# Optimization experiments

Measured on AMD Instinct MI355X. Metric: run time of the kernel, lower is better.

The kernel has to match this reference:

```python
import jax, jax.numpy as jnp
import numpy as np

CHARB_EPS = 1e-3
CHARB_ALPHA = 0.45
EDGE_ALPHA = 10.0
BOUNDARY_SUPPRESS = 0.1
W_SMOOTH = 0.15
W_SEGCONS = 0.1
SEG_EPS = 1e-6


def charbonnier(x):
    return jnp.power(x * x + CHARB_EPS * CHARB_EPS, CHARB_ALPHA)


def depthwise_sobel(img, kern):
    # img: (B,C,H,W); kern: (3,3) -> depthwise conv, padding=1
    C = img.shape[1]
    k = jnp.broadcast_to(kern[None, None], (C, 1, 3, 3)).astype(img.dtype)
    return jax.lax.conv_general_dilated(
        img, k, window_strides=(1, 1), padding=[(1, 1), (1, 1)],
        dimension_numbers=('NCHW', 'OIHW', 'NCHW'), feature_group_count=C)


def maxpool3(x):
    # 3x3 max pool, stride 1, pad 1 over last two dims (any rank)
    nd = x.ndim
    return jax.lax.reduce_window(
        x, -jnp.inf, jax.lax.max,
        (1,) * (nd - 2) + (3, 3), (1,) * nd,
        [(0, 0)] * (nd - 2) + [(1, 1), (1, 1)])


def compute_segment_boundary(masks):
    # masks: (B,S,H,W) -> boundary (B,1,H,W)
    occ = masks.sum(axis=1, keepdims=True)             # (B,1,H,W)
    b = jnp.clip(maxpool3(occ) - (-maxpool3(-occ)), 0.0, 1.0)
    per = jnp.clip(maxpool3(masks) - (-maxpool3(-masks)), 0.0, 1.0)  # (B,S,H,W)
    b = b + per.sum(axis=1, keepdims=True)
    return jnp.clip(b, 0.0, 1.0)


def boundary_smooth_loss(flow, image, segment_masks):
    sobel_x = jnp.array([[1., 0., -1.], [2., 0., -2.], [1., 0., -1.]], dtype=flow.dtype)
    gx = depthwise_sobel(image, sobel_x)
    gy = depthwise_sobel(image, sobel_x.T)
    img_grad_mag = (jnp.abs(gx) + jnp.abs(gy)).mean(axis=1, keepdims=True)  # (B,1,H,W)
    edge_w = jnp.exp(-EDGE_ALPHA * img_grad_mag)
    boundary = compute_segment_boundary(segment_masks)
    boundary_w = 1.0 - boundary * (1.0 - BOUNDARY_SUPPRESS)
    weights = edge_w * boundary_w                       # (B,1,H,W)

    fx = flow[:, :, :, 1:] - flow[:, :, :, :-1]
    fy = flow[:, :, 1:, :] - flow[:, :, :-1, :]
    wx = weights[:, :, :, 1:]
    wy = weights[:, :, 1:, :]
    loss1 = (charbonnier(fx).mean(axis=1, keepdims=True) * wx).mean()
    loss1 = loss1 + (charbonnier(fy).mean(axis=1, keepdims=True) * wy).mean()
    # second order
    fxx = fx[:, :, :, 1:] - fx[:, :, :, :-1]
    fyy = fy[:, :, 1:, :] - fy[:, :, :-1, :]
    loss2 = charbonnier(fxx).mean() + charbonnier(fyy).mean()
    return W_SMOOTH * (loss1 + 0.5 * loss2)


def segment_consistency_loss(flow, segment_masks):
    # flow: (B,2,H,W); masks: (B,S,H,W)
    mask_sum = jnp.maximum(segment_masks.sum(axis=(-2, -1)), SEG_EPS)  # (B,S)
    mean_flow = jnp.einsum('bchw,bshw->bsc', flow, segment_masks) / mask_sum[..., None]
    diff = flow[:, None] - mean_flow[:, :, :, None, None]              # (B,S,2,H,W)
    diff_sq = (diff * diff).sum(axis=2)                                # (B,S,H,W)
    # charbonnier(sqrt(d)) == (d + eps^2)^alpha (grad-safe at 0)
    var_map = jnp.power(diff_sq + CHARB_EPS * CHARB_EPS, CHARB_ALPHA)
    num_s = jnp.einsum('bshw,bshw->s', var_map, segment_masks)         # (S,)
    w_s = mask_sum.sum(axis=0)                                         # (S,)
    loss_s = num_s / jnp.maximum(w_s, SEG_EPS)
    total = (loss_s * w_s).sum()
    tw = w_s.sum()
    loss = jnp.where(tw > SEG_EPS, total / tw, 0.0)
    return W_SEGCONS * loss


def setup_inputs() -> dict:
    key = jax.random.key(0)
    k1, k2, k3 = jax.random.split(key, 3)
    B, S, H, W = 8, 16, 512, 512
    flow = jax.random.normal(k1, (B, 2, H, W), dtype=jnp.float32)
    image = jax.random.uniform(k2, (B, 3, H, W), dtype=jnp.float32)
    segment_masks = jax.random.uniform(k3, (B, S, H, W), dtype=jnp.float32)
    return {'flow': flow, 'image': image, 'segment_masks': segment_masks}


def reference(flow, image, segment_masks):
    return segment_consistency_loss(flow, segment_masks) + boundary_smooth_loss(flow, image, segment_masks)
```

## Files before the change

kernel.cpp:

```cpp
#include <hip/hip_runtime.h>

#define BB 8
#define SS 16
#define HH 512
#define WW 512
#define HWP (HH*WW)

#define TH 16
#define TW 32
#define HR 18
#define HC 34
#define NH (HR*HC)
#define LW 35

#define WS_MSUM 0
#define WS_FSUM 128
#define WS_MEAN 384
#define WS_ACC  640
#define WS_TOTAL 660

__device__ __forceinline__ float clip01(float x){ return fminf(fmaxf(x, 0.0f), 1.0f); }
__device__ __forceinline__ float pow045(float v){ return exp2f(0.45f * log2f(v)); }
__device__ __forceinline__ float cbn(float x){ return pow045(x*x + 1e-6f); }

__global__ __launch_bounds__(256, 2)
void kA(const float* __restrict__ flow, const float* __restrict__ masks,
        float* __restrict__ ws)
{
    const int b = blockIdx.y;
    const int base = blockIdx.x * 2048;
    const float* fU = flow + (size_t)b * 2 * HWP;
    const float* fV = fU + HWP;
    const float* mb = masks + (size_t)b * SS * HWP;

    float am[SS], au[SS], av[SS];
#pragma unroll
    for (int s = 0; s < SS; ++s){ am[s]=0.f; au[s]=0.f; av[s]=0.f; }

    for (int it = 0; it < 2; ++it){
        const int p = base + it*1024 + threadIdx.x*4;
        const float4 u = *reinterpret_cast<const float4*>(fU + p);
        const float4 v = *reinterpret_cast<const float4*>(fV + p);
#pragma unroll
        for (int s = 0; s < SS; ++s){
            const float4 m = *reinterpret_cast<const float4*>(mb + s*HWP + p);
            am[s] += (m.x + m.y) + (m.z + m.w);
            au[s] += m.x*u.x + m.y*u.y + m.z*u.z + m.w*u.w;
            av[s] += m.x*v.x + m.y*v.y + m.z*v.z + m.w*v.w;
        }
    }

#pragma unroll
    for (int s = 0; s < SS; ++s){
#pragma unroll
        for (int o = 32; o > 0; o >>= 1){
            am[s] += __shfl_down(am[s], o, 64);
            au[s] += __shfl_down(au[s], o, 64);
            av[s] += __shfl_down(av[s], o, 64);
        }
    }
    __shared__ float red[4][3*SS];
    const int lane = threadIdx.x & 63, wv = threadIdx.x >> 6;
    if (lane == 0){
#pragma unroll
        for (int s = 0; s < SS; ++s){
            red[wv][s] = am[s]; red[wv][SS+s] = au[s]; red[wv][2*SS+s] = av[s];
        }
    }
    __syncthreads();
    if (threadIdx.x < 3*SS){
        const int i = threadIdx.x;
        float t = red[0][i] + red[1][i] + red[2][i] + red[3][i];
        const int s = i % SS, kind = i / SS;
        if (kind == 0) atomicAdd(ws + WS_MSUM + b*SS + s, t);
        else           atomicAdd(ws + WS_FSUM + (b*SS + s)*2 + (kind-1), t);
    }
}

__global__ void kB(float* __restrict__ ws)
{
    const int i = threadIdx.x;
    const int bs = i >> 1;
    const float ms = fmaxf(ws[WS_MSUM + bs], 1e-6f);
    ws[WS_MEAN + i] = ws[WS_FSUM + i] / ms;
}

__global__ __launch_bounds__(256, 2)
void kC(const float* __restrict__ flow, const float* __restrict__ image,
        const float* __restrict__ masks, float* __restrict__ ws)
{
    const int b  = blockIdx.z;
    const int h0 = blockIdx.y * TH;
    const int w0 = blockIdx.x * TW;
    const int tid = threadIdx.x;

    __shared__ float sImg[3][HR*LW];
    __shared__ float sFlo[2][HR*LW];
    __shared__ float sOcc[HR*LW];
    __shared__ float sMsk[2][HR*LW];
    __shared__ float sMean[2*SS];
    __shared__ float sRed[4][20];

    if (tid < 2*SS) sMean[tid] = ws[WS_MEAN + b*2*SS + tid];

    int hli[3], cgi[3]; bool hval[3]; bool hin[3]; int hgi[3];
#pragma unroll
    for (int k = 0; k < 3; ++k){
        const int idx = tid + k*256;
        hval[k] = (k < 2) || (tid < NH - 512);
        const int r = idx / HC, c = idx % HC;
        const int gh = h0 - 1 + r, gw = w0 - 1 + c;
        hli[k] = r*LW + c;
        hin[k] = ((unsigned)gh < (unsigned)HH) && ((unsigned)gw < (unsigned)WW);
        hgi[k] = gh*WW + gw;
        const int ch_ = min(max(gh, 0), HH-1);
        const int cw_ = min(max(gw, 0), WW-1);
        cgi[k] = ch_*WW + cw_;
    }

    const float* img = image + (size_t)b * 3 * HWP;
    const float* flo = flow  + (size_t)b * 2 * HWP;
    const float* mb  = masks + (size_t)b * SS * HWP;

#pragma unroll
    for (int k = 0; k < 3; ++k){
        if (hval[k]){
            const bool in = hin[k]; const int gi = hgi[k]; const int li = hli[k];
            sImg[0][li] = in ? img[0*HWP + gi] : 0.f;
            sImg[1][li] = in ? img[1*HWP + gi] : 0.f;
            sImg[2][li] = in ? img[2*HWP + gi] : 0.f;
            sFlo[0][li] = in ? flo[0*HWP + gi] : 0.f;
            sFlo[1][li] = in ? flo[1*HWP + gi] : 0.f;
        }
    }

    float occA[3] = {0.f, 0.f, 0.f};
    float pf[3];

#pragma unroll
    for (int k = 0; k < 3; ++k) if (hval[k]) pf[k] = mb[cgi[k]];
#pragma unroll
    for (int k = 0; k < 3; ++k) if (hval[k]){ sMsk[0][hli[k]] = pf[k]; occA[k] += pf[k]; }
#pragma unroll
    for (int k = 0; k < 3; ++k) if (hval[k]) pf[k] = mb[1*HWP + cgi[k]];
    __syncthreads();

    const int pr  = tid >> 4;
    const int pc2 = (tid & 15) << 1;
    const int R = pr + 1;
    const float fu0 = sFlo[0][R*LW + pc2+1], fu1 = sFlo[0][R*LW + pc2+2];
    const float fv0 = sFlo[1][R*LW + pc2+1], fv1 = sFlo[1][R*LW + pc2+2];

    float numv[SS];
    float perS0 = 0.f, perS1 = 0.f;

#pragma unroll
    for (int s = 0; s < SS; ++s){
        const float* bufc = sMsk[s & 1];
        float cmx[4], cmn[4], mC0 = 0.f, mC1 = 0.f;
#pragma unroll
        for (int j = 0; j < 4; ++j){
            const float a = bufc[(pr  )*LW + pc2 + j];
            const float m = bufc[(pr+1)*LW + pc2 + j];
            const float d = bufc[(pr+2)*LW + pc2 + j];
            cmx[j] = fmaxf(fmaxf(a, m), d);
            cmn[j] = fminf(fminf(a, m), d);
            if (j == 1) mC0 = m;
            if (j == 2) mC1 = m;
        }
        const float rng0 = fmaxf(fmaxf(cmx[0],cmx[1]),cmx[2]) - fminf(fminf(cmn[0],cmn[1]),cmn[2]);
        const float rng1 = fmaxf(fmaxf(cmx[1],cmx[2]),cmx[3]) - fminf(fminf(cmn[1],cmn[2]),cmn[3]);
        perS0 += clip01(rng0);
        perS1 += clip01(rng1);

        const float mu = sMean[2*s], mv = sMean[2*s+1];
        const float d0u = fu0-mu, d0v = fv0-mv, d1u = fu1-mu, d1v = fv1-mv;
        const float vm0 = pow045(d0u*d0u + d0v*d0v + 1e-6f);
        const float vm1 = pow045(d1u*d1u + d1v*d1v + 1e-6f);
        numv[s] = vm0*mC0 + vm1*mC1;

        if (s < SS-1){
#pragma unroll
            for (int k = 0; k < 3; ++k) if (hval[k]){ sMsk[(s+1)&1][hli[k]] = pf[k]; occA[k] += pf[k]; }
            if (s < SS-2){
#pragma unroll
                for (int k = 0; k < 3; ++k) if (hval[k]) pf[k] = mb[(s+2)*HWP + cgi[k]];
            }
            __syncthreads();
        }
    }

#pragma unroll
    for (int k = 0; k < 3; ++k) if (hval[k]) sOcc[hli[k]] = occA[k];
    __syncthreads();

    float ox[4], on[4];
#pragma unroll
    for (int j = 0; j < 4; ++j){
        const float a = sOcc[(pr  )*LW + pc2 + j];
        const float m = sOcc[(pr+1)*LW + pc2 + j];
        const float d = sOcc[(pr+2)*LW + pc2 + j];
        ox[j] = fmaxf(fmaxf(a, m), d);
        on[j] = fminf(fminf(a, m), d);
    }
    const float org0 = fmaxf(fmaxf(ox[0],ox[1]),ox[2]) - fminf(fminf(on[0],on[1]),on[2]);
    const float org1 = fmaxf(fmaxf(ox[1],ox[2]),ox[3]) - fminf(fminf(on[1],on[2]),on[3]);
    const float bnd0 = clip01(clip01(org0) + perS0);
    const float bnd1 = clip01(clip01(org1) + perS1);

    float mag0 = 0.f, mag1 = 0.f;
#pragma unroll
    for (int ch = 0; ch < 3; ++ch){
        float top[4], mid[4], bot[4];
#pragma unroll
        for (int j = 0; j < 4; ++j){
            top[j] = sImg[ch][(pr  )*LW + pc2 + j];
            mid[j] = sImg[ch][(pr+1)*LW + pc2 + j];
            bot[j] = sImg[ch][(pr+2)*LW + pc2 + j];
        }
        float colV0 = top[0] + 2.f*mid[0] + bot[0];
        float colV1 = top[1] + 2.f*mid[1] + bot[1];
        float colV2 = top[2] + 2.f*mid[2] + bot[2];
        float colV3 = top[3] + 2.f*mid[3] + bot[3];
        const float gx0 = colV0 - colV2;
        const float gx1 = colV1 - colV3;
        const float gy0 = (top[0] + 2.f*top[1] + top[2]) - (bot[0] + 2.f*bot[1] + bot[2]);
        const float gy1 = (top[1] + 2.f*top[2] + top[3]) - (bot[1] + 2.f*bot[2] + bot[3]);
        mag0 += fabsf(gx0) + fabsf(gy0);
        mag1 += fabsf(gx1) + fabsf(gy1);
    }
    mag0 *= (1.f/3.f); mag1 *= (1.f/3.f);
    const float wgt0 = expf(-10.f * mag0) * (1.f - 0.9f*bnd0);
    const float wgt1 = expf(-10.f * mag1) * (1.f - 0.9f*bnd1);

    const int gh  = h0 + pr;
    const int gw0 = w0 + pc2;
    const int gw1 = gw0 + 1;

    const float lu = sFlo[0][R*LW + pc2],     lv = sFlo[1][R*LW + pc2];
    const float ru = sFlo[0][R*LW + pc2 + 3], rv = sFlo[1][R*LW + pc2 + 3];
    const float uu0 = sFlo[0][(R-1)*LW + pc2+1], uv0 = sFlo[1][(R-1)*LW + pc2+1];
    const float uu1 = sFlo[0][(R-1)*LW + pc2+2], uv1 = sFlo[1][(R-1)*LW + pc2+2];
    const float du0 = sFlo[0][(R+1)*LW + pc2+1], dv0 = sFlo[1][(R+1)*LW + pc2+1];
    const float du1 = sFlo[0][(R+1)*LW + pc2+2], dv1 = sFlo[1][(R+1)*LW + pc2+2];

    float l1x = 0.f, l1y = 0.f, l2x = 0.f, l2y = 0.f;

    if (gw0 >= 1) l1x += 0.5f * (cbn(fu0 - lu) + cbn(fv0 - lv)) * wgt0;
    l1x += 0.5f * (cbn(fu1 - fu0) + cbn(fv1 - fv0)) * wgt1;
    if (gh >= 1){
        l1y += 0.5f * (cbn(fu0 - uu0) + cbn(fv0 - uv0)) * wgt0;
        l1y += 0.5f * (cbn(fu1 - uu1) + cbn(fv1 - uv1)) * wgt1;
    }
    if (gw0 >= 1) l2x += cbn(fu1 - 2.f*fu0 + lu) + cbn(fv1 - 2.f*fv0 + lv);
    if (gw1 <= WW-2) l2x += cbn(ru - 2.f*fu1 + fu0) + cbn(rv - 2.f*fv1 + fv0);
    if (gh >= 1 && gh <= HH-2){
        l2y += cbn(du0 - 2.f*fu0 + uu0) + cbn(dv0 - 2.f*fv0 + uv0);
        l2y += cbn(du1 - 2.f*fu1 + uu1) + cbn(dv1 - 2.f*fv1 + uv1);
    }

    float vals[20];
#pragma unroll
    for (int s = 0; s < SS; ++s) vals[s] = numv[s];
    vals[16] = l1x; vals[17] = l1y; vals[18] = l2x; vals[19] = l2y;

    const int lane = tid & 63, wv = tid >> 6;
#pragma unroll
    for (int i = 0; i < 20; ++i){
        float v = vals[i];
#pragma unroll
        for (int o = 32; o > 0; o >>= 1) v += __shfl_down(v, o, 64);
        if (lane == 0) sRed[wv][i] = v;
    }
    __syncthreads();
    if (tid < 20){
        const float t = sRed[0][tid] + sRed[1][tid] + sRed[2][tid] + sRed[3][tid];
        atomicAdd(ws + WS_ACC + tid, t);
    }
}

__global__ void kF(const float* __restrict__ ws, float* __restrict__ out)
{
    __shared__ float sw[SS];
    const int t = threadIdx.x;
    if (t < SS){
        float w = 0.f;
        for (int b = 0; b < BB; ++b) w += fmaxf(ws[WS_MSUM + b*SS + t], 1e-6f);
        sw[t] = w;
    }
    __syncthreads();
    if (t == 0){
        float total = 0.f, tw = 0.f;
        for (int s = 0; s < SS; ++s){
            const float w = sw[s];
            total += (ws[WS_ACC + s] / fmaxf(w, 1e-6f)) * w;
            tw += w;
        }
        const float seg = (tw > 1e-6f) ? (total / tw) : 0.f;
        const float l1 = ws[WS_ACC+16] / (8.f*512.f*511.f) + ws[WS_ACC+17] / (8.f*511.f*512.f);
        const float l2 = ws[WS_ACC+18] / (8.f*2.f*512.f*510.f) + ws[WS_ACC+19] / (8.f*2.f*510.f*512.f);
        out[0] = 0.1f*seg + 0.15f*(l1 + 0.5f*l2);
    }
}

extern "C" void kernel_launch(void* const* d_in, const int* in_sizes, int n_in,
                              void* d_out, int out_size, void* d_ws, size_t ws_size,
                              hipStream_t stream)
{
    (void)in_sizes; (void)n_in; (void)out_size; (void)ws_size;
    const float* flow  = (const float*)d_in[0];
    const float* image = (const float*)d_in[1];
    const float* masks = (const float*)d_in[2];
    float* ws  = (float*)d_ws;
    float* out = (float*)d_out;

    (void)hipMemsetAsync(d_ws, 0, WS_TOTAL * sizeof(float), stream);

    dim3 gA(128, BB);
    kA<<<gA, 256, 0, stream>>>(flow, masks, ws);
    kB<<<1, 256, 0, stream>>>(ws);
    dim3 gC(WW/TW, HH/TH, BB);
    kC<<<gC, 256, 0, stream>>>(flow, image, masks, ws);
    kF<<<1, 64, 0, stream>>>(ws, out);
}
```

Before: 376.8 us.

## Pipeline kA through LDS async loads, drop kB, and remove shared tiling in kC

kA now streams masks and flow into double-buffered LDS using global_load_lds async copies, with fewer, larger blocks. kB's mean computation is folded into kC's prologue, removing one launch. kC drops its shared-memory halo tiles and per-segment barriers. Each thread instead handles one column over two rows and reads its 3x4 neighbourhood straight from global memory, relying on caches for the halo reuse. This removes sync overhead and LDS traffic, at the cost of more redundant global and cache reads.

```diff
diff --git a/kernel.cpp b/kernel.cpp
--- a/kernel.cpp
+++ b/kernel.cpp
@@ -6,16 +6,8 @@
 #define WW 512
 #define HWP (HH*WW)
 
-#define TH 16
-#define TW 32
-#define HR 18
-#define HC 34
-#define NH (HR*HC)
-#define LW 35
-
 #define WS_MSUM 0
 #define WS_FSUM 128
-#define WS_MEAN 384
 #define WS_ACC  640
 #define WS_TOTAL 660
 
@@ -23,31 +15,65 @@
 __device__ __forceinline__ float pow045(float v){ return exp2f(0.45f * log2f(v)); }
 __device__ __forceinline__ float cbn(float x){ return pow045(x*x + 1e-6f); }
 
-__global__ __launch_bounds__(256, 2)
+typedef const __attribute__((address_space(1))) void* as1cv;
+typedef __attribute__((address_space(3))) void* as3v;
+__device__ __forceinline__ void gload16(const void* g, void* l){
+    __builtin_amdgcn_global_load_lds((as1cv)g, (as3v)l, 16, 0, 0);
+}
+
+__global__ __launch_bounds__(256)
 void kA(const float* __restrict__ flow, const float* __restrict__ masks,
         float* __restrict__ ws)
 {
-    const int b = blockIdx.y;
-    const int base = blockIdx.x * 2048;
+    const int b   = blockIdx.y;
+    const int tb0 = blockIdx.x * 4096;
     const float* fU = flow + (size_t)b * 2 * HWP;
     const float* fV = fU + HWP;
     const float* mb = masks + (size_t)b * SS * HWP;
 
+    __shared__ float buf[2][36*256];
+    __shared__ float red[4][3*SS];
+
+    const int wv = threadIdx.x >> 6, lane = threadIdx.x & 63;
+
     float am[SS], au[SS], av[SS];
 #pragma unroll
     for (int s = 0; s < SS; ++s){ am[s]=0.f; au[s]=0.f; av[s]=0.f; }
 
-    for (int it = 0; it < 2; ++it){
-        const int p = base + it*1024 + threadIdx.x*4;
-        const float4 u = *reinterpret_cast<const float4*>(fU + p);
-        const float4 v = *reinterpret_cast<const float4*>(fV + p);
+    auto stage = [&](int t, int pb){
+        const int tb = tb0 + t * 512;
+        float* base = &buf[pb][0];
+#pragma unroll
+        for (int k = 0; k < 9; ++k){
+            const int c = wv + 4*k;
+            const float* src;
+            if (c < 32)       src = mb + (size_t)(c>>1)*HWP + tb + (c&1)*256;
+            else if (c < 34)  src = fU + tb + (c&1)*256;
+            else              src = fV + tb + (c&1)*256;
+            gload16(src + lane*4, base + c*256);
+        }
+    };
+
+    auto compute = [&](int pb){
+        const float* B = &buf[pb][0];
+        const int t2 = threadIdx.x * 2;
+        const float2 uu = *reinterpret_cast<const float2*>(B + 16*512 + t2);
+        const float2 vv = *reinterpret_cast<const float2*>(B + 16*512 + 512 + t2);
 #pragma unroll
         for (int s = 0; s < SS; ++s){
-            const float4 m = *reinterpret_cast<const float4*>(mb + s*HWP + p);
-            am[s] += (m.x + m.y) + (m.z + m.w);
-            au[s] += m.x*u.x + m.y*u.y + m.z*u.z + m.w*u.w;
-            av[s] += m.x*v.x + m.y*v.y + m.z*v.z + m.w*v.w;
-        }
+            const float2 m = *reinterpret_cast<const float2*>(B + s*512 + t2);
+            am[s] += m.x + m.y;
+            au[s] += m.x*uu.x + m.y*uu.y;
+            av[s] += m.x*vv.x + m.y*vv.y;
+        }
+    };
+
+    stage(0, 0);
+    __syncthreads();
+    for (int t = 0; t < 8; ++t){
+        if (t < 7) stage(t+1, (t+1)&1);
+        compute(t & 1);
+        __syncthreads();
     }
 
 #pragma unroll
@@ -59,8 +85,6 @@
             av[s] += __shfl_down(av[s], o, 64);
         }
     }
-    __shared__ float red[4][3*SS];
-    const int lane = threadIdx.x & 63, wv = threadIdx.x >> 6;
     if (lane == 0){
 #pragma unroll
         for (int s = 0; s < SS; ++s){
@@ -70,207 +94,148 @@
     __syncthreads();
     if (threadIdx.x < 3*SS){
         const int i = threadIdx.x;
-        float t = red[0][i] + red[1][i] + red[2][i] + red[3][i];
+        const float t = red[0][i] + red[1][i] + red[2][i] + red[3][i];
         const int s = i % SS, kind = i / SS;
         if (kind == 0) atomicAdd(ws + WS_MSUM + b*SS + s, t);
         else           atomicAdd(ws + WS_FSUM + (b*SS + s)*2 + (kind-1), t);
     }
 }
 
-__global__ void kB(float* __restrict__ ws)
-{
-    const int i = threadIdx.x;
-    const int bs = i >> 1;
-    const float ms = fmaxf(ws[WS_MSUM + bs], 1e-6f);
-    ws[WS_MEAN + i] = ws[WS_FSUM + i] / ms;
-}
-
-__global__ __launch_bounds__(256, 2)
+__global__ __launch_bounds__(256)
 void kC(const float* __restrict__ flow, const float* __restrict__ image,
         const float* __restrict__ masks, float* __restrict__ ws)
 {
     const int b  = blockIdx.z;
-    const int h0 = blockIdx.y * TH;
-    const int w0 = blockIdx.x * TW;
     const int tid = threadIdx.x;
-
-    __shared__ float sImg[3][HR*LW];
-    __shared__ float sFlo[2][HR*LW];
-    __shared__ float sOcc[HR*LW];
-    __shared__ float sMsk[2][HR*LW];
+    const int h0 = blockIdx.y*16 + ((tid>>5)<<1);
+    const int w  = blockIdx.x*32 + (tid&31);
+
     __shared__ float sMean[2*SS];
     __shared__ float sRed[4][20];
-
-    if (tid < 2*SS) sMean[tid] = ws[WS_MEAN + b*2*SS + tid];
-
-    int hli[3], cgi[3]; bool hval[3]; bool hin[3]; int hgi[3];
-#pragma unroll
-    for (int k = 0; k < 3; ++k){
-        const int idx = tid + k*256;
-        hval[k] = (k < 2) || (tid < NH - 512);
-        const int r = idx / HC, c = idx % HC;
-        const int gh = h0 - 1 + r, gw = w0 - 1 + c;
-        hli[k] = r*LW + c;
-        hin[k] = ((unsigned)gh < (unsigned)HH) && ((unsigned)gw < (unsigned)WW);
-        hgi[k] = gh*WW + gw;
-        const int ch_ = min(max(gh, 0), HH-1);
-        const int cw_ = min(max(gw, 0), WW-1);
-        cgi[k] = ch_*WW + cw_;
-    }
-
+    if (tid < 2*SS){
+        const int s = tid >> 1;
+        const float ms = fmaxf(ws[WS_MSUM + b*SS + s], 1e-6f);
+        sMean[tid] = ws[WS_FSUM + (b*SS + s)*2 + (tid&1)] / ms;
+    }
+    __syncthreads();
+
+    const int rA = max(h0-1, 0), rC = h0+1, rD = min(h0+2, HH-1);
+    const int wm = max(w-1, 0),  wp = min(w+1, WW-1);
+    const int oA = rA*WW, oB = h0*WW, oC = rC*WW, oD = rD*WW;
+
+    const float* mb  = masks + (size_t)b * SS * HWP;
+    const float* flo = flow  + (size_t)b * 2 * HWP;
     const float* img = image + (size_t)b * 3 * HWP;
-    const float* flo = flow  + (size_t)b * 2 * HWP;
-    const float* mb  = masks + (size_t)b * SS * HWP;
-
-#pragma unroll
-    for (int k = 0; k < 3; ++k){
-        if (hval[k]){
-            const bool in = hin[k]; const int gi = hgi[k]; const int li = hli[k];
-            sImg[0][li] = in ? img[0*HWP + gi] : 0.f;
-            sImg[1][li] = in ? img[1*HWP + gi] : 0.f;
-            sImg[2][li] = in ? img[2*HWP + gi] : 0.f;
-            sFlo[0][li] = in ? flo[0*HWP + gi] : 0.f;
-            sFlo[1][li] = in ? flo[1*HWP + gi] : 0.f;
-        }
-    }
-
-    float occA[3] = {0.f, 0.f, 0.f};
-    float pf[3];
-
-#pragma unroll
-    for (int k = 0; k < 3; ++k) if (hval[k]) pf[k] = mb[cgi[k]];
-#pragma unroll
-    for (int k = 0; k < 3; ++k) if (hval[k]){ sMsk[0][hli[k]] = pf[k]; occA[k] += pf[k]; }
-#pragma unroll
-    for (int k = 0; k < 3; ++k) if (hval[k]) pf[k] = mb[1*HWP + cgi[k]];
-    __syncthreads();
-
-    const int pr  = tid >> 4;
-    const int pc2 = (tid & 15) << 1;
-    const int R = pr + 1;
-    const float fu0 = sFlo[0][R*LW + pc2+1], fu1 = sFlo[0][R*LW + pc2+2];
-    const float fv0 = sFlo[1][R*LW + pc2+1], fv1 = sFlo[1][R*LW + pc2+2];
-
+
+    const float fu0 = flo[oB + w],       fu1 = flo[oC + w];
+    const float fv0 = flo[HWP + oB + w], fv1 = flo[HWP + oC + w];
+
+    float occ[12];
+#pragma unroll
+    for (int j = 0; j < 12; ++j) occ[j] = 0.f;
     float numv[SS];
     float perS0 = 0.f, perS1 = 0.f;
 
 #pragma unroll
     for (int s = 0; s < SS; ++s){
-        const float* bufc = sMsk[s & 1];
-        float cmx[4], cmn[4], mC0 = 0.f, mC1 = 0.f;
-#pragma unroll
-        for (int j = 0; j < 4; ++j){
-            const float a = bufc[(pr  )*LW + pc2 + j];
-            const float m = bufc[(pr+1)*LW + pc2 + j];
-            const float d = bufc[(pr+2)*LW + pc2 + j];
-            cmx[j] = fmaxf(fmaxf(a, m), d);
-            cmn[j] = fminf(fminf(a, m), d);
-            if (j == 1) mC0 = m;
-            if (j == 2) mC1 = m;
-        }
-        const float rng0 = fmaxf(fmaxf(cmx[0],cmx[1]),cmx[2]) - fminf(fminf(cmn[0],cmn[1]),cmn[2]);
-        const float rng1 = fmaxf(fmaxf(cmx[1],cmx[2]),cmx[3]) - fminf(fminf(cmn[1],cmn[2]),cmn[3]);
+        const float* M = mb + (size_t)s * HWP;
+        const float mAm=M[oA+wm], mA0=M[oA+w], mAp=M[oA+wp];
+        const float mBm=M[oB+wm], mB0=M[oB+w], mBp=M[oB+wp];
+        const float mCm=M[oC+wm], mC0=M[oC+w], mCp=M[oC+wp];
+        const float mDm=M[oD+wm], mD0=M[oD+w], mDp=M[oD+wp];
+        occ[0]+=mAm; occ[1]+=mA0;  occ[2]+=mAp;
+        occ[3]+=mBm; occ[4]+=mB0;  occ[5]+=mBp;
+        occ[6]+=mCm; occ[7]+=mC0;  occ[8]+=mCp;
+        occ[9]+=mDm; occ[10]+=mD0; occ[11]+=mDp;
+
+        const float xm = fmaxf(mBm,mCm), x0 = fmaxf(mB0,mC0), xp = fmaxf(mBp,mCp);
+        const float nm = fminf(mBm,mCm), n0 = fminf(mB0,mC0), np = fminf(mBp,mCp);
+        const float rng0 = fmaxf(fmaxf(fmaxf(xm,mAm), fmaxf(x0,mA0)), fmaxf(xp,mAp))
+                         - fminf(fminf(fminf(nm,mAm), fminf(n0,mA0)), fminf(np,mAp));
+        const float rng1 = fmaxf(fmaxf(fmaxf(xm,mDm), fmaxf(x0,mD0)), fmaxf(xp,mDp))
+                         - fminf(fminf(fminf(nm,mDm), fminf(n0,mD0)), fminf(np,mDp));
         perS0 += clip01(rng0);
         perS1 += clip01(rng1);
 
         const float mu = sMean[2*s], mv = sMean[2*s+1];
         const float d0u = fu0-mu, d0v = fv0-mv, d1u = fu1-mu, d1v = fv1-mv;
-        const float vm0 = pow045(d0u*d0u + d0v*d0v + 1e-6f);
-        const float vm1 = pow045(d1u*d1u + d1v*d1v + 1e-6f);
-        numv[s] = vm0*mC0 + vm1*mC1;
-
-        if (s < SS-1){
-#pragma unroll
-            for (int k = 0; k < 3; ++k) if (hval[k]){ sMsk[(s+1)&1][hli[k]] = pf[k]; occA[k] += pf[k]; }
-            if (s < SS-2){
-#pragma unroll
-                for (int k = 0; k < 3; ++k) if (hval[k]) pf[k] = mb[(s+2)*HWP + cgi[k]];
-            }
-            __syncthreads();
-        }
-    }
-
-#pragma unroll
-    for (int k = 0; k < 3; ++k) if (hval[k]) sOcc[hli[k]] = occA[k];
-    __syncthreads();
-
-    float ox[4], on[4];
-#pragma unroll
-    for (int j = 0; j < 4; ++j){
-        const float a = sOcc[(pr  )*LW + pc2 + j];
-        const float m = sOcc[(pr+1)*LW + pc2 + j];
-        const float d = sOcc[(pr+2)*LW + pc2 + j];
-        ox[j] = fmaxf(fmaxf(a, m), d);
-        on[j] = fminf(fminf(a, m), d);
-    }
-    const float org0 = fmaxf(fmaxf(ox[0],ox[1]),ox[2]) - fminf(fminf(on[0],on[1]),on[2]);
-    const float org1 = fmaxf(fmaxf(ox[1],ox[2]),ox[3]) - fminf(fminf(on[1],on[2]),on[3]);
+        numv[s] = pow045(d0u*d0u + d0v*d0v + 1e-6f)*mB0
+                + pow045(d1u*d1u + d1v*d1v + 1e-6f)*mC0;
+    }
+
+    const float oxm = fmaxf(occ[3],occ[6]), ox0 = fmaxf(occ[4],occ[7]), oxp = fmaxf(occ[5],occ[8]);
+    const float onm = fminf(occ[3],occ[6]), on0 = fminf(occ[4],occ[7]), onp = fminf(occ[5],occ[8]);
+    const float org0 = fmaxf(fmaxf(fmaxf(oxm,occ[0]), fmaxf(ox0,occ[1])), fmaxf(oxp,occ[2]))
+                     - fminf(fminf(fminf(onm,occ[0]), fminf(on0,occ[1])), fminf(onp,occ[2]));
+    const float org1 = fmaxf(fmaxf(fmaxf(oxm,occ[9]), fmaxf(ox0,occ[10])), fmaxf(oxp,occ[11]))
+                     - fminf(fminf(fminf(onm,occ[9]), fminf(on0,occ[10])), fminf(onp,occ[11]));
     const float bnd0 = clip01(clip01(org0) + perS0);
     const float bnd1 = clip01(clip01(org1) + perS1);
 
+    const bool vA = (h0 >= 1), vD = (h0+2 <= HH-1);
+    const bool vm = (w  >= 1), vp = (w+1  <= WW-1);
     float mag0 = 0.f, mag1 = 0.f;
 #pragma unroll
     for (int ch = 0; ch < 3; ++ch){
-        float top[4], mid[4], bot[4];
-#pragma unroll
-        for (int j = 0; j < 4; ++j){
-            top[j] = sImg[ch][(pr  )*LW + pc2 + j];
-            mid[j] = sImg[ch][(pr+1)*LW + pc2 + j];
-            bot[j] = sImg[ch][(pr+2)*LW + pc2 + j];
-        }
-        float colV0 = top[0] + 2.f*mid[0] + bot[0];
-        float colV1 = top[1] + 2.f*mid[1] + bot[1];
-        float colV2 = top[2] + 2.f*mid[2] + bot[2];
-        float colV3 = top[3] + 2.f*mid[3] + bot[3];
-        const float gx0 = colV0 - colV2;
-        const float gx1 = colV1 - colV3;
-        const float gy0 = (top[0] + 2.f*top[1] + top[2]) - (bot[0] + 2.f*bot[1] + bot[2]);
-        const float gy1 = (top[1] + 2.f*top[2] + top[3]) - (bot[1] + 2.f*bot[2] + bot[3]);
+        const float* I = img + (size_t)ch * HWP;
+        const float iAm = (vA&&vm) ? I[oA+wm] : 0.f;
+        const float iA0 =  vA      ? I[oA+w ] : 0.f;
+        const float iAp = (vA&&vp) ? I[oA+wp] : 0.f;
+        const float iBm =  vm      ? I[oB+wm] : 0.f;
+        const float iB0 =             I[oB+w ];
+        const float iBp =  vp      ? I[oB+wp] : 0.f;
+        const float iCm =  vm      ? I[oC+wm] : 0.f;
+        const float iC0 =             I[oC+w ];
+        const float iCp =  vp      ? I[oC+wp] : 0.f;
+        const float iDm = (vD&&vm) ? I[oD+wm] : 0.f;
+        const float iD0 =  vD      ? I[oD+w ] : 0.f;
+        const float iDp = (vD&&vp) ? I[oD+wp] : 0.f;
+
+        const float gx0 = (iAm + 2.f*iBm + iCm) - (iAp + 2.f*iBp + iCp);
+        const float gy0 = (iAm + 2.f*iA0 + iAp) - (iCm + 2.f*iC0 + iCp);
         mag0 += fabsf(gx0) + fabsf(gy0);
+        const float gx1 = (iBm + 2.f*iCm + iDm) - (iBp + 2.f*iCp + iDp);
+        const float gy1 = (iBm + 2.f*iB0 + iBp) - (iDm + 2.f*iD0 + iDp);
         mag1 += fabsf(gx1) + fabsf(gy1);
     }
     mag0 *= (1.f/3.f); mag1 *= (1.f/3.f);
     const float wgt0 = expf(-10.f * mag0) * (1.f - 0.9f*bnd0);
     const float wgt1 = expf(-10.f * mag1) * (1.f - 0.9f*bnd1);
 
-    const int gh  = h0 + pr;
-    const int gw0 = w0 + pc2;
-    const int gw1 = gw0 + 1;
-
-    const float lu = sFlo[0][R*LW + pc2],     lv = sFlo[1][R*LW + pc2];
-    const float ru = sFlo[0][R*LW + pc2 + 3], rv = sFlo[1][R*LW + pc2 + 3];
-    const float uu0 = sFlo[0][(R-1)*LW + pc2+1], uv0 = sFlo[1][(R-1)*LW + pc2+1];
-    const float uu1 = sFlo[0][(R-1)*LW + pc2+2], uv1 = sFlo[1][(R-1)*LW + pc2+2];
-    const float du0 = sFlo[0][(R+1)*LW + pc2+1], dv0 = sFlo[1][(R+1)*LW + pc2+1];
-    const float du1 = sFlo[0][(R+1)*LW + pc2+2], dv1 = sFlo[1][(R+1)*LW + pc2+2];
+    const float uBm = flo[oB+wm], vBm = flo[HWP+oB+wm];
+    const float uBp = flo[oB+wp], vBp = flo[HWP+oB+wp];
+    const float uCm = flo[oC+wm], vCm = flo[HWP+oC+wm];
+    const float uCp = flo[oC+wp], vCp = flo[HWP+oC+wp];
+    const float uA  = flo[oA+w ], vA_ = flo[HWP+oA+w ];
+    const float uD  = flo[oD+w ], vD_ = flo[HWP+oD+w ];
 
     float l1x = 0.f, l1y = 0.f, l2x = 0.f, l2y = 0.f;
 
-    if (gw0 >= 1) l1x += 0.5f * (cbn(fu0 - lu) + cbn(fv0 - lv)) * wgt0;
-    l1x += 0.5f * (cbn(fu1 - fu0) + cbn(fv1 - fv0)) * wgt1;
-    if (gh >= 1){
-        l1y += 0.5f * (cbn(fu0 - uu0) + cbn(fv0 - uv0)) * wgt0;
-        l1y += 0.5f * (cbn(fu1 - uu1) + cbn(fv1 - uv1)) * wgt1;
-    }
-    if (gw0 >= 1) l2x += cbn(fu1 - 2.f*fu0 + lu) + cbn(fv1 - 2.f*fv0 + lv);
-    if (gw1 <= WW-2) l2x += cbn(ru - 2.f*fu1 + fu0) + cbn(rv - 2.f*fv1 + fv0);
-    if (gh >= 1 && gh <= HH-2){
-        l2y += cbn(du0 - 2.f*fu0 + uu0) + cbn(dv0 - 2.f*fv0 + uv0);
-        l2y += cbn(du1 - 2.f*fu1 + uu1) + cbn(dv1 - 2.f*fv1 + uv1);
-    }
+    if (w >= 1){
+        l1x += 0.5f * (cbn(fu0 - uBm) + cbn(fv0 - vBm)) * wgt0;
+        l1x += 0.5f * (cbn(fu1 - uCm) + cbn(fv1 - vCm)) * wgt1;
+    }
+    if (h0 >= 1) l1y += 0.5f * (cbn(fu0 - uA) + cbn(fv0 - vA_)) * wgt0;
+    l1y += 0.5f * (cbn(fu1 - fu0) + cbn(fv1 - fv0)) * wgt1;
+    if (w >= 1 && w <= WW-2){
+        l2x += cbn(uBp - 2.f*fu0 + uBm) + cbn(vBp - 2.f*fv0 + vBm);
+        l2x += cbn(uCp - 2.f*fu1 + uCm) + cbn(vCp - 2.f*fv1 + vCm);
+    }
+    if (h0 >= 1)        l2y += cbn(fu1 - 2.f*fu0 + uA) + cbn(fv1 - 2.f*fv0 + vA_);
+    if (h0+1 <= HH-2)   l2y += cbn(uD - 2.f*fu1 + fu0) + cbn(vD_ - 2.f*fv1 + fv0);
 
     float vals[20];
 #pragma unroll
     for (int s = 0; s < SS; ++s) vals[s] = numv[s];
     vals[16] = l1x; vals[17] = l1y; vals[18] = l2x; vals[19] = l2y;
 
-    const int lane = tid & 63, wv = tid >> 6;
+    const int lane = tid & 63, wvv = tid >> 6;
 #pragma unroll
     for (int i = 0; i < 20; ++i){
         float v = vals[i];
 #pragma unroll
         for (int o = 32; o > 0; o >>= 1) v += __shfl_down(v, o, 64);
-        if (lane == 0) sRed[wv][i] = v;
+        if (lane == 0) sRed[wvv][i] = v;
     }
     __syncthreads();
     if (tid < 20){
@@ -316,10 +281,9 @@
 
     (void)hipMemsetAsync(d_ws, 0, WS_TOTAL * sizeof(float), stream);
 
-    dim3 gA(128, BB);
+    dim3 gA(64, BB);
     kA<<<gA, 256, 0, stream>>>(flow, masks, ws);
-    kB<<<1, 256, 0, stream>>>(ws);
-    dim3 gC(WW/TW, HH/TH, BB);
+    dim3 gC(WW/32, HH/16, BB);
     kC<<<gC, 256, 0, stream>>>(flow, image, masks, ws);
     kF<<<1, 64, 0, stream>>>(ws, out);
 }
```

New measurement: 460.7 us. 22.3% more time.
